# Optimization experiments

Measured on AMD Instinct MI355X. Metric: run time of the kernel, lower is better.

The kernel has to match this reference:

```python
import jax, jax.numpy as jnp
import numpy as np

B, N, D = 32, 2048, 1024


def setup_inputs() -> dict:
    key0 = jax.random.key(0)
    ks = jax.random.split(key0, 9)
    scale = 1.0 / np.sqrt(D)
    query = jax.random.normal(ks[0], (B, D), dtype=jnp.float32)
    key = jax.random.normal(ks[1], (B, N, D), dtype=jnp.float32)
    mask = jax.random.randint(ks[2], (B, N), 0, 2, dtype=jnp.int32)
    W1 = jax.random.uniform(ks[3], (D, D), jnp.float32, -scale, scale)
    b1 = jax.random.uniform(ks[4], (D,), jnp.float32, -scale, scale)
    W2 = jax.random.uniform(ks[5], (D, D), jnp.float32, -scale, scale)
    b2 = jax.random.uniform(ks[6], (D,), jnp.float32, -scale, scale)
    v_w = jax.random.uniform(ks[7], (D,), jnp.float32, -scale, scale)
    v_b = jax.random.uniform(ks[8], (), jnp.float32, -scale, scale)
    return {"query": query, "key": key, "mask": mask,
            "W1": W1, "b1": b1, "W2": W2, "b2": b2, "v_w": v_w, "v_b": v_b}


def reference(query, key, mask, W1, b1, W2, b2, v_w, v_b):
    # key_out: [B, N, D] = key @ W1^T + b1 (nn.Linear convention)
    key_out = jnp.einsum('bnd,ed->bne', key, W1) + b1
    # query_out: [B, D] -> broadcast over N
    query_out = jnp.einsum('bd,ed->be', query, W2) + b2
    h = jnp.tanh(key_out + query_out[:, None, :])  # [B, N, D]
    ui = jnp.einsum('bnd,d->bn', h, v_w) + v_b      # v: D -> 1, squeezed
    ui = jnp.where(mask.astype(bool), ui, -jnp.inf)
    return ui
```

## Files before the change

### kernel.cpp

```cpp
#include <hip/hip_runtime.h>
#include <hip/hip_bf16.h>
#include <math.h>

#define B_ 32
#define N_ 2048
#define D_ 1024
#define M_ (B_ * N_)

typedef float  fx4  __attribute__((ext_vector_type(4)));
typedef float  fx2  __attribute__((ext_vector_type(2)));
typedef __bf16 bf16x8 __attribute__((ext_vector_type(8)));
typedef unsigned short us4 __attribute__((ext_vector_type(4)));

#define WS_T 2097152ULL

#define MASK_NEG_SENTINEL (-1.0e30f)

__device__ inline unsigned short f2b(float f) {
    __hip_bfloat16 h = __float2bfloat16(f);
    return *reinterpret_cast<unsigned short*>(&h);
}

__global__ void w1_convert_kernel(const fx4* __restrict__ W1,
                                  us4* __restrict__ w1b4) {
    int idx = blockIdx.x * blockDim.x + threadIdx.x;
#pragma unroll
    for (int i = 0; i < 4; ++i) {
        int j = idx + i * 65536;
        fx4 v = W1[j];
        us4 o; o.x = f2b(v.x); o.y = f2b(v.y); o.z = f2b(v.z); o.w = f2b(v.w);
        w1b4[j] = o;
    }
}

__global__ void tq_kernel(const float* __restrict__ query,
                          const float* __restrict__ W2,
                          const float* __restrict__ b1,
                          const float* __restrict__ b2,
                          float* __restrict__ t) {
    int tid = threadIdx.x;
    int p = blockIdx.x * 32 + (tid >> 3);
    int j = tid & 7;
    int b = p >> 10;
    int e = p & 1023;
    const fx4* q = (const fx4*)query + (size_t)b * 256;
    const fx4* w = (const fx4*)W2 + (size_t)e * 256;
    float acc = 0.f;
#pragma unroll 4
    for (int it = 0; it < 32; ++it) {
        int k4 = it * 8 + j;
        fx4 qv = q[k4];
        fx4 wv = w[k4];
        acc += qv.x * wv.x + qv.y * wv.y + qv.z * wv.z + qv.w * wv.w;
    }
    acc += __shfl_xor(acc, 1);
    acc += __shfl_xor(acc, 2);
    acc += __shfl_xor(acc, 4);
    if (j == 0) t[p] = acc + b1[e] + b2[e];
}

__device__ inline float fast_tanh(float x) {
    float ax = fabsf(x);
    float e  = __expf(-2.0f * ax);
    float r  = (1.0f - e) / (1.0f + e);
    return copysignf(r, x);
}

#define BM 64
#define BK 32

#define GLD16(g, l)                                                        \
    __builtin_amdgcn_global_load_lds(                                      \
        (const __attribute__((address_space(1))) void*)(g),                \
        (__attribute__((address_space(3))) void*)(l), 16, 0, 0)

__global__ void __launch_bounds__(1024, 4)
fused_main(const float* __restrict__ key,
           const unsigned short* __restrict__ w1b,
           const float* __restrict__ t,
           const float* __restrict__ v_w,
           const float* __restrict__ v_b,
           const int* __restrict__ mask,
           float* __restrict__ out) {
    __shared__ unsigned short Bs[2][D_ * BK];
    __shared__ unsigned short As[2][BM * BK];
    __shared__ float rs[16][BM];

    const int tid  = threadIdx.x;
    const int lane = tid & 63;
    const int wave = tid >> 6;
    const int quad = lane >> 4;
    const int l15  = lane & 15;
    const int m0   = blockIdx.x * BM;

    const int sB  = (lane & 7) ^ (lane >> 3);
    const int eL  = ((lane >> 3) << 1) | (sB >> 2);
    const int ksB = sB & 3;
    const unsigned short* bsrc =
        w1b + (size_t)(wave * 64 + eL) * D_ + ksB * 8;

    const int arow = tid >> 4;
    const int akk  = tid & 15;
    const float* asrc = key + (size_t)(m0 + arow) * D_ + akk * 2;
    const int aP  = arow >> 1;
    const int asl = (((arow & 1) << 2) | (akk >> 2)) ^ (aP & 7);
    const int aDstOff = aP * 128 + asl * 16 + (akk & 3) * 4;

    int aOff[4], bOff[4];
#pragma unroll
    for (int i = 0; i < 4; ++i) {
        int row = i * 16 + l15;
        aOff[i] = (row >> 1) * 128 +
                  ((((row & 1) << 2) | quad) ^ ((row >> 1) & 7)) * 16;
    }
#pragma unroll
    for (int j = 0; j < 4; ++j) {
        int e = wave * 64 + j * 16 + l15;
        bOff[j] = (e >> 1) * 128 +
                  ((((e & 1) << 2) | quad) ^ ((e >> 1) & 7)) * 16;
    }

    fx4 acc[4][4] = {};

    {
        char* bd = (char*)Bs[0] + wave * 4096;
#pragma unroll
        for (int q = 0; q < 4; ++q)
            GLD16(bsrc + q * 16 * D_, bd + q * 1024);
        fx2 v = *(const fx2*)asrc;
        unsigned int pk = f2b(v.x) | ((unsigned int)f2b(v.y) << 16);
        *(unsigned int*)((char*)As[0] + aDstOff) = pk;
    }
    __syncthreads();

    int cur = 0;
    for (int tt = 0; tt < 32; ++tt) {
        const int k0n = (tt + 1) * BK;
        fx2 vA;
        const bool pf = (tt < 31);
        if (pf) {
            char* bd = (char*)Bs[cur ^ 1] + wave * 4096;
#pragma unroll
            for (int q = 0; q < 4; ++q)
                GLD16(bsrc + q * 16 * D_ + k0n, bd + q * 1024);
            vA = *(const fx2*)(asrc + k0n);
        }

        bf16x8 a[4], b[4];
#pragma unroll
        for (int i = 0; i < 4; ++i)
            a[i] = *(const bf16x8*)((const char*)As[cur] + aOff[i]);
#pragma unroll
        for (int j = 0; j < 4; ++j)
            b[j] = *(const bf16x8*)((const char*)Bs[cur] + bOff[j]);
#pragma unroll
        for (int i = 0; i < 4; ++i)
#pragma unroll
            for (int j = 0; j < 4; ++j)
                acc[i][j] = __builtin_amdgcn_mfma_f32_16x16x32_bf16(
                    a[i], b[j], acc[i][j], 0, 0, 0);

        if (pf) {
            unsigned int pk = f2b(vA.x) | ((unsigned int)f2b(vA.y) << 16);
            *(unsigned int*)((char*)As[cur ^ 1] + aDstOff) = pk;
        }
        __syncthreads();
        cur ^= 1;
    }

    const float* trow = t + (size_t)(m0 >> 11) * D_;
    float vwv[4], tqv[4];
#pragma unroll
    for (int j = 0; j < 4; ++j) {
        int e = wave * 64 + j * 16 + l15;
        vwv[j] = v_w[e];
        tqv[j] = trow[e];
    }
#pragma unroll
    for (int i = 0; i < 4; ++i)
#pragma unroll
        for (int r = 0; r < 4; ++r) {
            float s = 0.f;
#pragma unroll
            for (int j = 0; j < 4; ++j)
                s += vwv[j] * fast_tanh(acc[i][j][r] + tqv[j]);
            s += __shfl_xor(s, 1);
            s += __shfl_xor(s, 2);
            s += __shfl_xor(s, 4);
            s += __shfl_xor(s, 8);
            if (l15 == 0) rs[wave][i * 16 + quad * 4 + r] = s;
        }
    __syncthreads();

    if (tid < BM) {
        float u = 0.f;
#pragma unroll
        for (int w = 0; w < 16; ++w) u += rs[w][tid];
        const int m = m0 + tid;
        out[m] = mask[m] ? (u + v_b[0]) : MASK_NEG_SENTINEL;
    }
}

extern "C" void kernel_launch(void* const* d_in, const int* in_sizes, int n_in,
                              void* d_out, int out_size, void* d_ws, size_t ws_size,
                              hipStream_t stream) {
    const float* query = (const float*)d_in[0];
    const float* key   = (const float*)d_in[1];
    const int*   mask  = (const int*)d_in[2];
    const float* W1    = (const float*)d_in[3];
    const float* b1    = (const float*)d_in[4];
    const float* W2    = (const float*)d_in[5];
    const float* b2    = (const float*)d_in[6];
    const float* v_w   = (const float*)d_in[7];
    const float* v_b   = (const float*)d_in[8];

    char* ws = (char*)d_ws;
    unsigned short* w1b = (unsigned short*)ws;
    float*          t   = (float*)(ws + WS_T);

    w1_convert_kernel<<<256, 256, 0, stream>>>((const fx4*)W1, (us4*)w1b);
    tq_kernel<<<1024, 256, 0, stream>>>(query, W2, b1, b2, t);
    fused_main<<<M_ / BM, 1024, 0, stream>>>(key, w1b, t, v_w, v_b, mask,
                                             (float*)d_out);
}
```

Before: 618.1 us.

## Deepen GEMM main-loop pipeline with manual waitcnt, register prefetch and peeled tail

Splits the double-buffered LDS tiles into named buffers and rewrites the K loop. The key (A) tile is now prefetched into registers two steps ahead, and `__syncthreads` is replaced by explicit `s_waitcnt` counters plus raw barriers. This lets the async W1 loads for the next tile overlap the MFMAs without full drains. It also raises wave priority around the MFMA block and peels the last two iterations. The aim is to hide global-load latency in the fused GEMM+tanh kernel. The cost is fragile hand-tuned vmcnt accounting that depends on the exact load ordering the compiler emits.

Result: faster. 600.3 us (-2.9%).

```diff
diff --git a/kernel.cpp b/kernel.cpp
--- a/kernel.cpp
+++ b/kernel.cpp
@@ -82,8 +82,10 @@
            const float* __restrict__ v_b,
            const int* __restrict__ mask,
            float* __restrict__ out) {
-    __shared__ unsigned short Bs[2][D_ * BK];
-    __shared__ unsigned short As[2][BM * BK];
+    __shared__ unsigned short Bs0[D_ * BK];
+    __shared__ unsigned short Bs1[D_ * BK];
+    __shared__ unsigned short As0[BM * BK];
+    __shared__ unsigned short As1[BM * BK];
     __shared__ float rs[16][BM];
 
     const int tid  = threadIdx.x;
@@ -121,51 +123,102 @@
     }
 
     fx4 acc[4][4] = {};
+    fx2 aNext;
 
     {
-        char* bd = (char*)Bs[0] + wave * 4096;
+        char* bd = (char*)Bs0 + wave * 4096;
 #pragma unroll
         for (int q = 0; q < 4; ++q)
             GLD16(bsrc + q * 16 * D_, bd + q * 1024);
-        fx2 v = *(const fx2*)asrc;
-        unsigned int pk = f2b(v.x) | ((unsigned int)f2b(v.y) << 16);
-        *(unsigned int*)((char*)As[0] + aDstOff) = pk;
-    }
-    __syncthreads();
-
-    int cur = 0;
-    for (int tt = 0; tt < 32; ++tt) {
-        const int k0n = (tt + 1) * BK;
-        fx2 vA;
-        const bool pf = (tt < 31);
-        if (pf) {
-            char* bd = (char*)Bs[cur ^ 1] + wave * 4096;
-#pragma unroll
-            for (int q = 0; q < 4; ++q)
-                GLD16(bsrc + q * 16 * D_ + k0n, bd + q * 1024);
-            vA = *(const fx2*)(asrc + k0n);
-        }
-
+        fx2 v0 = *(const fx2*)asrc;
+        aNext   = *(const fx2*)(asrc + BK);
+        unsigned int pk = f2b(v0.x) | ((unsigned int)f2b(v0.y) << 16);
+        *(unsigned int*)((char*)As0 + aDstOff) = pk;
+        asm volatile("s_waitcnt lgkmcnt(0)" ::: "memory");
+        __builtin_amdgcn_s_barrier();
+        asm volatile("" ::: "memory");
+    }
+
+#pragma unroll 2
+    for (int tt = 0; tt < 30; ++tt) {
+        const int p = tt & 1;
+        const unsigned short* BsP = p ? Bs1 : Bs0;
+        unsigned short*       BsQ = p ? Bs0 : Bs1;
+        const unsigned short* AsP = p ? As1 : As0;
+        unsigned short*       AsQ = p ? As0 : As1;
+
+        char* bd = (char*)BsQ + wave * 4096;
+#pragma unroll
+        for (int q = 0; q < 4; ++q)
+            GLD16(bsrc + q * 16 * D_ + (size_t)(tt + 1) * BK, bd + q * 1024);
+        fx2 aFut = *(const fx2*)(asrc + (size_t)(tt + 2) * BK);
+        unsigned int pk = f2b(aNext.x) | ((unsigned int)f2b(aNext.y) << 16);
+        *(unsigned int*)((char*)AsQ + aDstOff) = pk;
+        asm volatile("s_waitcnt vmcnt(6)" ::: "memory");
         bf16x8 a[4], b[4];
 #pragma unroll
         for (int i = 0; i < 4; ++i)
-            a[i] = *(const bf16x8*)((const char*)As[cur] + aOff[i]);
+            a[i] = *(const bf16x8*)((const char*)AsP + aOff[i]);
 #pragma unroll
         for (int j = 0; j < 4; ++j)
-            b[j] = *(const bf16x8*)((const char*)Bs[cur] + bOff[j]);
+            b[j] = *(const bf16x8*)((const char*)BsP + bOff[j]);
+        __builtin_amdgcn_s_setprio(1);
 #pragma unroll
         for (int i = 0; i < 4; ++i)
 #pragma unroll
             for (int j = 0; j < 4; ++j)
                 acc[i][j] = __builtin_amdgcn_mfma_f32_16x16x32_bf16(
                     a[i], b[j], acc[i][j], 0, 0, 0);
-
-        if (pf) {
-            unsigned int pk = f2b(vA.x) | ((unsigned int)f2b(vA.y) << 16);
-            *(unsigned int*)((char*)As[cur ^ 1] + aDstOff) = pk;
-        }
-        __syncthreads();
-        cur ^= 1;
+        __builtin_amdgcn_s_setprio(0);
+        aNext = aFut;
+        asm volatile("s_waitcnt lgkmcnt(0)" ::: "memory");
+        __builtin_amdgcn_s_barrier();
+        asm volatile("" ::: "memory");
+    }
+
+    {
+        char* bd = (char*)Bs1 + wave * 4096;
+#pragma unroll
+        for (int q = 0; q < 4; ++q)
+            GLD16(bsrc + q * 16 * D_ + (size_t)31 * BK, bd + q * 1024);
+        unsigned int pk = f2b(aNext.x) | ((unsigned int)f2b(aNext.y) << 16);
+        *(unsigned int*)((char*)As1 + aDstOff) = pk;
+        asm volatile("s_waitcnt vmcnt(4)" ::: "memory");
+        bf16x8 a[4], b[4];
+#pragma unroll
+        for (int i = 0; i < 4; ++i)
+            a[i] = *(const bf16x8*)((const char*)As0 + aOff[i]);
+#pragma unroll
+        for (int j = 0; j < 4; ++j)
+            b[j] = *(const bf16x8*)((const char*)Bs0 + bOff[j]);
+        __builtin_amdgcn_s_setprio(1);
+#pragma unroll
+        for (int i = 0; i < 4; ++i)
+#pragma unroll
+            for (int j = 0; j < 4; ++j)
+                acc[i][j] = __builtin_amdgcn_mfma_f32_16x16x32_bf16(
+                    a[i], b[j], acc[i][j], 0, 0, 0);
+        __builtin_amdgcn_s_setprio(0);
+        asm volatile("s_waitcnt lgkmcnt(0)" ::: "memory");
+        __builtin_amdgcn_s_barrier();
+        asm volatile("" ::: "memory");
+    }
+    {
+        asm volatile("s_waitcnt vmcnt(0)" ::: "memory");
+        __builtin_amdgcn_sched_barrier(0);
+        bf16x8 a[4], b[4];
+#pragma unroll
+        for (int i = 0; i < 4; ++i)
+            a[i] = *(const bf16x8*)((const char*)As1 + aOff[i]);
+#pragma unroll
+        for (int j = 0; j < 4; ++j)
+            b[j] = *(const bf16x8*)((const char*)Bs1 + bOff[j]);
+#pragma unroll
+        for (int i = 0; i < 4; ++i)
+#pragma unroll
+            for (int j = 0; j < 4; ++j)
+                acc[i][j] = __builtin_amdgcn_mfma_f32_16x16x32_bf16(
+                    a[i], b[j], acc[i][j], 0, 0, 0);
     }
 
     const float* trow = t + (size_t)(m0 >> 11) * D_;
```

## Split output columns across two blocks with atomic reduction and deeper A prefetch

Applied to the files above, without the earlier changes.

Each block now covers only half of the D output columns (512 threads instead of 1024), so the grid doubles. Partial v-dot sums are combined by atomicAdd into a zeroed workspace, and a finalize kernel applies the mask and bias. The key rows are loaded as float4 and prefetched three tiles ahead with explicit vmcnt waits, raw barriers and setprio around the MFMAs. The aim is better occupancy and latency hiding, at the cost of re-reading each key tile twice, plus the atomics, a memset and an extra launch.

After: 577.4 us. -6.6%, faster.

```diff
diff --git a/kernel.cpp b/kernel.cpp
--- a/kernel.cpp
+++ b/kernel.cpp
@@ -8,11 +8,11 @@
 #define M_ (B_ * N_)
 
 typedef float  fx4  __attribute__((ext_vector_type(4)));
-typedef float  fx2  __attribute__((ext_vector_type(2)));
 typedef __bf16 bf16x8 __attribute__((ext_vector_type(8)));
 typedef unsigned short us4 __attribute__((ext_vector_type(4)));
 
-#define WS_T 2097152ULL
+#define WS_T   2097152ULL
+#define WS_ACC 2228224ULL
 
 #define MASK_NEG_SENTINEL (-1.0e30f)
 
@@ -74,37 +74,42 @@
         (const __attribute__((address_space(1))) void*)(g),                \
         (__attribute__((address_space(3))) void*)(l), 16, 0, 0)
 
-__global__ void __launch_bounds__(1024, 4)
+__global__ void __launch_bounds__(512, 4)
 fused_main(const float* __restrict__ key,
            const unsigned short* __restrict__ w1b,
            const float* __restrict__ t,
            const float* __restrict__ v_w,
-           const float* __restrict__ v_b,
-           const int* __restrict__ mask,
-           float* __restrict__ out) {
-    __shared__ unsigned short Bs[2][D_ * BK];
-    __shared__ unsigned short As[2][BM * BK];
-    __shared__ float rs[16][BM];
+           float* __restrict__ accum) {
+    __shared__ unsigned short Bs0[512 * BK];
+    __shared__ unsigned short Bs1[512 * BK];
+    __shared__ unsigned short As0[BM * BK];
+    __shared__ unsigned short As1[BM * BK];
+    __shared__ float rs[8][BM];
 
     const int tid  = threadIdx.x;
     const int lane = tid & 63;
     const int wave = tid >> 6;
     const int quad = lane >> 4;
     const int l15  = lane & 15;
-    const int m0   = blockIdx.x * BM;
+
+    const int p_   = blockIdx.x;
+    const int mt   = (p_ >> 4) * 8 + (p_ & 7);
+    const int hh   = (p_ >> 3) & 1;
+    const int m0   = mt * BM;
+    const int eb   = hh * 512;
 
     const int sB  = (lane & 7) ^ (lane >> 3);
     const int eL  = ((lane >> 3) << 1) | (sB >> 2);
     const int ksB = sB & 3;
     const unsigned short* bsrc =
-        w1b + (size_t)(wave * 64 + eL) * D_ + ksB * 8;
-
-    const int arow = tid >> 4;
-    const int akk  = tid & 15;
-    const float* asrc = key + (size_t)(m0 + arow) * D_ + akk * 2;
+        w1b + (size_t)(eb + wave * 64 + eL) * D_ + ksB * 8;
+
+    const int arow = tid >> 3;
+    const int akq  = tid & 7;
+    const float* asrc = key + (size_t)(m0 + arow) * D_ + akq * 4;
     const int aP  = arow >> 1;
-    const int asl = (((arow & 1) << 2) | (akk >> 2)) ^ (aP & 7);
-    const int aDstOff = aP * 128 + asl * 16 + (akk & 3) * 4;
+    const int asl = (((arow & 1) << 2) | (akq >> 1)) ^ (aP & 7);
+    const int aDstOff = aP * 128 + asl * 16 + (akq & 1) * 8;
 
     int aOff[4], bOff[4];
 #pragma unroll
@@ -121,58 +126,68 @@
     }
 
     fx4 acc[4][4] = {};
+    fx4 aN1, aN2;
 
     {
-        char* bd = (char*)Bs[0] + wave * 4096;
+        char* bd = (char*)Bs0 + wave * 4096;
 #pragma unroll
         for (int q = 0; q < 4; ++q)
             GLD16(bsrc + q * 16 * D_, bd + q * 1024);
-        fx2 v = *(const fx2*)asrc;
-        unsigned int pk = f2b(v.x) | ((unsigned int)f2b(v.y) << 16);
-        *(unsigned int*)((char*)As[0] + aDstOff) = pk;
-    }
-    __syncthreads();
-
-    int cur = 0;
+        fx4 v0 = *(const fx4*)asrc;
+        aN1 = *(const fx4*)(asrc + BK);
+        aN2 = *(const fx4*)(asrc + 2 * BK);
+        us4 o; o.x = f2b(v0.x); o.y = f2b(v0.y);
+        o.z = f2b(v0.z); o.w = f2b(v0.w);
+        *(us4*)((char*)As0 + aDstOff) = o;
+        asm volatile("s_waitcnt lgkmcnt(0)" ::: "memory");
+        __builtin_amdgcn_s_barrier();
+        asm volatile("" ::: "memory");
+    }
+
     for (int tt = 0; tt < 32; ++tt) {
-        const int k0n = (tt + 1) * BK;
-        fx2 vA;
-        const bool pf = (tt < 31);
-        if (pf) {
-            char* bd = (char*)Bs[cur ^ 1] + wave * 4096;
-#pragma unroll
-            for (int q = 0; q < 4; ++q)
-                GLD16(bsrc + q * 16 * D_ + k0n, bd + q * 1024);
-            vA = *(const fx2*)(asrc + k0n);
-        }
-
+        const int par = tt & 1;
+        const unsigned short* BsP = par ? Bs1 : Bs0;
+        unsigned short*       BsQ = par ? Bs0 : Bs1;
+        const unsigned short* AsP = par ? As1 : As0;
+        unsigned short*       AsQ = par ? As0 : As1;
+
+        int kb = tt + 1; if (kb > 31) kb = 31;
+        char* bd = (char*)BsQ + wave * 4096;
+#pragma unroll
+        for (int q = 0; q < 4; ++q)
+            GLD16(bsrc + q * 16 * D_ + (size_t)kb * BK, bd + q * 1024);
+        int ka = tt + 3; if (ka > 31) ka = 31;
+        fx4 aFut = *(const fx4*)(asrc + (size_t)ka * BK);
+        us4 o; o.x = f2b(aN1.x); o.y = f2b(aN1.y);
+        o.z = f2b(aN1.z); o.w = f2b(aN1.w);
+        *(us4*)((char*)AsQ + aDstOff) = o;
+        aN1 = aN2; aN2 = aFut;
+        asm volatile("s_waitcnt vmcnt(6)" ::: "memory");
         bf16x8 a[4], b[4];
 #pragma unroll
         for (int i = 0; i < 4; ++i)
-            a[i] = *(const bf16x8*)((const char*)As[cur] + aOff[i]);
+            a[i] = *(const bf16x8*)((const char*)AsP + aOff[i]);
 #pragma unroll
         for (int j = 0; j < 4; ++j)
-            b[j] = *(const bf16x8*)((const char*)Bs[cur] + bOff[j]);
+            b[j] = *(const bf16x8*)((const char*)BsP + bOff[j]);
+        __builtin_amdgcn_s_setprio(1);
 #pragma unroll
         for (int i = 0; i < 4; ++i)
 #pragma unroll
             for (int j = 0; j < 4; ++j)
                 acc[i][j] = __builtin_amdgcn_mfma_f32_16x16x32_bf16(
                     a[i], b[j], acc[i][j], 0, 0, 0);
-
-        if (pf) {
-            unsigned int pk = f2b(vA.x) | ((unsigned int)f2b(vA.y) << 16);
-            *(unsigned int*)((char*)As[cur ^ 1] + aDstOff) = pk;
-        }
-        __syncthreads();
-        cur ^= 1;
+        __builtin_amdgcn_s_setprio(0);
+        asm volatile("s_waitcnt lgkmcnt(0)" ::: "memory");
+        __builtin_amdgcn_s_barrier();
+        asm volatile("" ::: "memory");
     }
 
     const float* trow = t + (size_t)(m0 >> 11) * D_;
     float vwv[4], tqv[4];
 #pragma unroll
     for (int j = 0; j < 4; ++j) {
-        int e = wave * 64 + j * 16 + l15;
+        int e = eb + wave * 64 + j * 16 + l15;
         vwv[j] = v_w[e];
         tqv[j] = trow[e];
     }
@@ -195,9 +210,19 @@
     if (tid < BM) {
         float u = 0.f;
 #pragma unroll
-        for (int w = 0; w < 16; ++w) u += rs[w][tid];
-        const int m = m0 + tid;
-        out[m] = mask[m] ? (u + v_b[0]) : MASK_NEG_SENTINEL;
+        for (int w = 0; w < 8; ++w) u += rs[w][tid];
+        atomicAdd(&accum[m0 + tid], u);
+    }
+}
+
+__global__ void finalize_kernel(const float* __restrict__ accum,
+                                const int* __restrict__ mask,
+                                const float* __restrict__ v_b,
+                                float* __restrict__ out) {
+    int i = blockIdx.x * blockDim.x + threadIdx.x;
+    if (i < M_) {
+        float vb = v_b[0];
+        out[i] = mask[i] ? (accum[i] + vb) : MASK_NEG_SENTINEL;
     }
 }
 
@@ -217,9 +242,12 @@
     char* ws = (char*)d_ws;
     unsigned short* w1b = (unsigned short*)ws;
     float*          t   = (float*)(ws + WS_T);
+    float*          acc = (float*)(ws + WS_ACC);
 
     w1_convert_kernel<<<256, 256, 0, stream>>>((const fx4*)W1, (us4*)w1b);
     tq_kernel<<<1024, 256, 0, stream>>>(query, W2, b1, b2, t);
-    fused_main<<<M_ / BM, 1024, 0, stream>>>(key, w1b, t, v_w, v_b, mask,
-                                             (float*)d_out);
-}
+    hipMemsetAsync(acc, 0, (size_t)M_ * sizeof(float), stream);
+    fused_main<<<2048, 512, 0, stream>>>(key, w1b, t, v_w, acc);
+    finalize_kernel<<<M_ / 256, 256, 0, stream>>>(acc, mask, v_b,
+                                                  (float*)d_out);
+}
```
